# Kernel tuning notes

Measured on AMD Instinct MI355X. Metric: run time of the kernel, lower is better.

The kernel has to match this reference:

```python
import jax, jax.numpy as jnp
import numpy as np

B, S, P, E, H, FF = 4, 16, 256, 768, 12, 3072
HD = E // H
LN_EPS = 1e-5


def _layernorm(x, g, b):
    m = jnp.mean(x, axis=-1, keepdims=True)
    v = jnp.mean((x - m) ** 2, axis=-1, keepdims=True)
    return (x - m) * jax.lax.rsqrt(v + LN_EPS) * g + b


def _qkv(x, wqkv, bqkv):
    # wqkv: [3, E, E] (in, out layout), bqkv: [3, E]
    qkv = jnp.einsum('bspe,tef->tbspf', x, wqkv) + bqkv[:, None, None, None, :]
    q, k, v = qkv
    b, s, p, e = x.shape
    shp = (b, s, p, H, HD)
    return q.reshape(shp), k.reshape(shp), v.reshape(shp)


def spatial_attn(x, wqkv, bqkv, wo, bo, g, beta):
    q, k, v = _qkv(x, wqkv, bqkv)  # [b,s,p,n,d]
    scale = 1.0 / np.sqrt(HD).astype(np.float32)
    scores = jnp.einsum('bsind,bsjnd->bsnij', q, k) * scale  # [b,s,n,p,p]
    attn = jax.nn.softmax(scores, axis=-1)
    out = jnp.einsum('bsnij,bsjnd->bsind', attn, v)  # [b,s,p,n,d]
    out = out.reshape(x.shape)
    out = out @ wo + bo
    return _layernorm(x + out, g, beta)


def temporal_attn(x, wqkv, bqkv, wo, bo, g, beta):
    q, k, v = _qkv(x, wqkv, bqkv)  # [b,s,p,n,d]
    scale = 1.0 / np.sqrt(HD).astype(np.float32)
    scores = jnp.einsum('bipnd,bjpnd->bpnij', q, k) * scale  # [b,p,n,s,s]
    s = x.shape[1]
    causal = jnp.tril(jnp.ones((s, s), dtype=bool))
    scores = jnp.where(causal, scores, jnp.float32(-jnp.inf))
    attn = jax.nn.softmax(scores, axis=-1)
    out = jnp.einsum('bpnij,bjpnd->bipnd', attn, v)  # [b,s,p,n,d]
    out = out.reshape(x.shape)
    out = out @ wo + bo
    return _layernorm(x + out, g, beta)


def ffn(x, w1, b1, w2, b2, g, beta):
    h = jax.nn.relu(x @ w1 + b1)
    out = h @ w2 + b2
    return _layernorm(x + out, g, beta)


def setup_inputs() -> dict:
    key = jax.random.key(0)
    ks = jax.random.split(key, 16)
    w = lambda k, shp: (jax.random.normal(k, shp, dtype=jnp.float32) * 0.02)
    inp = {
        'x': jax.random.normal(ks[0], (B, S, P, E), dtype=jnp.float32),
        'sa_wqkv': w(ks[1], (3, E, E)), 'sa_bqkv': jnp.zeros((3, E), jnp.float32),
        'sa_wo': w(ks[2], (E, E)), 'sa_bo': jnp.zeros((E,), jnp.float32),
        'sa_g': jnp.ones((E,), jnp.float32), 'sa_b': jnp.zeros((E,), jnp.float32),
        'ta_wqkv': w(ks[3], (3, E, E)), 'ta_bqkv': jnp.zeros((3, E), jnp.float32),
        'ta_wo': w(ks[4], (E, E)), 'ta_bo': jnp.zeros((E,), jnp.float32),
        'ta_g': jnp.ones((E,), jnp.float32), 'ta_b': jnp.zeros((E,), jnp.float32),
        'f_w1': w(ks[5], (E, FF)), 'f_b1': jnp.zeros((FF,), jnp.float32),
        'f_w2': w(ks[6], (FF, E)), 'f_b2': jnp.zeros((E,), jnp.float32),
        'f_g': jnp.ones((E,), jnp.float32), 'f_b': jnp.zeros((E,), jnp.float32),
    }
    return inp


def reference(x, sa_wqkv, sa_bqkv, sa_wo, sa_bo, sa_g, sa_b,
              ta_wqkv, ta_bqkv, ta_wo, ta_bo, ta_g, ta_b,
              f_w1, f_b1, f_w2, f_b2, f_g, f_b):
    x = spatial_attn(x, sa_wqkv, sa_bqkv, sa_wo, sa_bo, sa_g, sa_b)
    x = temporal_attn(x, ta_wqkv, ta_bqkv, ta_wo, ta_bo, ta_g, ta_b)
    x = ffn(x, f_w1, f_b1, f_w2, f_b2, f_g, f_b)
    return x
```

## Files before the change

kernel.cpp:

```cpp
#include <hip/hip_runtime.h>
#include <hip/hip_bf16.h>
#include <math.h>

constexpr int Bc = 4, Sc = 16, Pc = 256, Ec = 768, Hc = 12, HDc = 64, FFc = 3072;
constexpr int Mrows = Bc * Sc * Pc;
constexpr size_t ME = (size_t)Mrows * Ec;

typedef __attribute__((ext_vector_type(4))) float f32x4;
typedef __attribute__((ext_vector_type(8))) short s16x8;
typedef __attribute__((ext_vector_type(4))) short s16x4;

__device__ __forceinline__ short f2bf(float f) {
  union { float f; unsigned u; } v; v.f = f;
  unsigned r = (v.u + 0x7FFFu + ((v.u >> 16) & 1u)) >> 16;
  return (short)r;
}
__device__ __forceinline__ float bf2f(short s) {
  union { unsigned u; float f; } v; v.u = ((unsigned)(unsigned short)s) << 16;
  return v.f;
}

__device__ __forceinline__ void async16(const void* g, void* l) {
  __builtin_amdgcn_global_load_lds(
      (const __attribute__((address_space(1))) unsigned int*)g,
      (__attribute__((address_space(3))) unsigned int*)l, 16, 0, 0);
}

__device__ __forceinline__ void wtrans_tile(const float* __restrict__ W,
                                            short* __restrict__ Wt,
                                            int K, int N, int n0, int k0, int t)
{
  const int n  = n0 + (t >> 2);
  const int kc = k0 + (t & 3) * 16;
  short buf[16];
#pragma unroll
  for (int i = 0; i < 16; ++i)
    buf[i] = f2bf(W[(size_t)(kc + i) * N + n]);
  *reinterpret_cast<s16x8*>(&Wt[(size_t)n * K + kc])     = *reinterpret_cast<s16x8*>(&buf[0]);
  *reinterpret_cast<s16x8*>(&Wt[(size_t)n * K + kc + 8]) = *reinterpret_cast<s16x8*>(&buf[8]);
}

__global__ __launch_bounds__(256)
void prep_kernel(const float* __restrict__ x, short* __restrict__ Xb,
                 const float* __restrict__ saqkv, short* __restrict__ wt_saqkv,
                 const float* __restrict__ sawo,  short* __restrict__ wt_sawo,
                 const float* __restrict__ taqkv, short* __restrict__ wt_taqkv,
                 const float* __restrict__ tawo,  short* __restrict__ wt_tawo,
                 const float* __restrict__ fw1,   short* __restrict__ wt_fw1,
                 const float* __restrict__ fw2,   short* __restrict__ wt_fw2)
{
  const int b = blockIdx.x;
  const int t = threadIdx.x;
  constexpr size_t EE = (size_t)Ec * Ec;

  if (b < 432) {
    const int z = b / 144, tl = b % 144;
    wtrans_tile(saqkv + (size_t)z * EE, wt_saqkv + (size_t)z * EE,
                Ec, Ec, (tl % 12) * 64, (tl / 12) * 64, t);
  } else if (b < 576) {
    const int tl = b - 432;
    wtrans_tile(sawo, wt_sawo, Ec, Ec, (tl % 12) * 64, (tl / 12) * 64, t);
  } else if (b < 1008) {
    const int z = (b - 576) / 144, tl = (b - 576) % 144;
    wtrans_tile(taqkv + (size_t)z * EE, wt_taqkv + (size_t)z * EE,
                Ec, Ec, (tl % 12) * 64, (tl / 12) * 64, t);
  } else if (b < 1152) {
    const int tl = b - 1008;
    wtrans_tile(tawo, wt_tawo, Ec, Ec, (tl % 12) * 64, (tl / 12) * 64, t);
  } else if (b < 1728) {
    const int tl = b - 1152;
    wtrans_tile(fw1, wt_fw1, Ec, FFc, (tl % 48) * 64, (tl / 48) * 64, t);
  } else if (b < 2304) {
    const int tl = b - 1728;
    wtrans_tile(fw2, wt_fw2, FFc, Ec, (tl % 12) * 64, (tl / 12) * 64, t);
  } else {
    const size_t i = (size_t)(b - 2304) * 256 + t;
    const float4* p = reinterpret_cast<const float4*>(x + i * 8);
    float4 a = p[0], bb = p[1];
    s16x8 o = { f2bf(a.x), f2bf(a.y), f2bf(a.z), f2bf(a.w),
                f2bf(bb.x), f2bf(bb.y), f2bf(bb.z), f2bf(bb.w) };
    *reinterpret_cast<s16x8*>(Xb + i * 8) = o;
  }
}

#define LDFRAG(base, row, kc) \
  (*reinterpret_cast<const s16x8*>((base) + (row) * 128 + ((((kc) ^ ((row) & 7)) << 4))))

#define PH_READS(Aslot, Bslot, q, LDB) \
  do { \
    if (LDB) { \
      _Pragma("unroll") \
      for (int nj = 0; nj < 4; ++nj) { \
        bfr[nj][0] = LDFRAG((Bslot), wc * 64 + nj * 16 + l16, g); \
        bfr[nj][1] = LDFRAG((Bslot), wc * 64 + nj * 16 + l16, 4 + g); \
      } \
    } \
    _Pragma("unroll") \
    for (int mi = 0; mi < 2; ++mi) { \
      const int arow = wr * 128 + ((q) * 2 + mi) * 16 + l16; \
      afr[mi][0] = LDFRAG((Aslot), arow, g); \
      afr[mi][1] = LDFRAG((Aslot), arow, 4 + g); \
    } \
  } while (0)

#define PH_SYNC_MMA(q) \
  do { \
    __builtin_amdgcn_sched_barrier(0); \
    __builtin_amdgcn_s_barrier(); \
    asm volatile("s_waitcnt lgkmcnt(0)" ::: "memory"); \
    __builtin_amdgcn_sched_barrier(0); \
    __builtin_amdgcn_s_setprio(1); \
    _Pragma("unroll") \
    for (int mi = 0; mi < 2; ++mi) \
      _Pragma("unroll") \
      for (int nj = 0; nj < 4; ++nj) { \
        acc[(q) * 2 + mi][nj] = __builtin_amdgcn_mfma_f32_16x16x32_bf16( \
            afr[mi][0], bfr[nj][0], acc[(q) * 2 + mi][nj], 0, 0, 0); \
        acc[(q) * 2 + mi][nj] = __builtin_amdgcn_mfma_f32_16x16x32_bf16( \
            afr[mi][1], bfr[nj][1], acc[(q) * 2 + mi][nj], 0, 0, 0); \
      } \
    __builtin_amdgcn_s_setprio(0); \
  } while (0)

#define PH_END \
  do { __builtin_amdgcn_s_barrier(); __builtin_amdgcn_sched_barrier(0); } while (0)

#define PH_END_VM \
  do { \
    asm volatile("s_waitcnt vmcnt(4)" ::: "memory"); \
    __builtin_amdgcn_sched_barrier(0); \
    __builtin_amdgcn_s_barrier(); \
    __builtin_amdgcn_sched_barrier(0); \
  } while (0)

template<int OUT>
__global__ __launch_bounds__(512, 2)
void gemm256_kernel(const short* __restrict__ A, const short* __restrict__ Wt,
                    const float* __restrict__ biasg, const void* __restrict__ resv,
                    void* __restrict__ Cg, short* __restrict__ vt,
                    int M, int N, int K)
{
  __shared__ char smem[131072];
  const int z = blockIdx.z;
  const short* __restrict__ Wz = Wt + (size_t)z * (size_t)N * K;
  const float* __restrict__ bz = biasg + (size_t)z * N;

  const int nwg = gridDim.x;
  const int swz = ((int)blockIdx.x & 7) * (nwg >> 3) + ((int)blockIdx.x >> 3);
  const int NT = N >> 8;
  const int bm = (swz / NT) << 8;
  const int bn = (swz % NT) << 8;

  const int tid  = threadIdx.x;
  const int lane = tid & 63;
  const int wid  = tid >> 6;
  const int wr   = wid >> 2;
  const int wc   = wid & 3;
  const int l16  = lane & 15;
  const int g    = lane >> 4;

  char* const As0 = smem;
  char* const Bs0 = smem + 32768;
  char* const As1 = smem + 65536;
  char* const Bs1 = smem + 98304;

  const int srow = lane >> 3;
  const int scol = ((lane & 7) ^ srow) * 8;
  const int ldso = wid * 1024;

  auto stageG = [&](const short* __restrict__ G, int grow0, int k0, char* ldsHalf) {
    const size_t r0 = (size_t)(grow0 + wid * 8 + srow);
    async16(G + r0 * K + (k0 + scol), ldsHalf + ldso);
    async16(G + (r0 + 64) * K + (k0 + scol), ldsHalf + 8192 + ldso);
  };

  f32x4 acc[8][4];
  s16x8 bfr[4][2];
  s16x8 afr[2][2];
#pragma unroll
  for (int mi = 0; mi < 8; ++mi)
#pragma unroll
    for (int nj = 0; nj < 4; ++nj) acc[mi][nj] = f32x4{0.f, 0.f, 0.f, 0.f};

  const int ntile = K >> 6;
  const int nit   = ntile >> 1;

  stageG(A,  bm,        0,  As0);
  stageG(A,  bm + 128,  0,  As0 + 16384);
  stageG(Wz, bn,        0,  Bs0);
  stageG(Wz, bn + 128,  0,  Bs0 + 16384);
  stageG(Wz, bn,        64, Bs1);
  stageG(Wz, bn + 128,  64, Bs1 + 16384);
  asm volatile("s_waitcnt vmcnt(4)" ::: "memory");
  __builtin_amdgcn_sched_barrier(0);
  __builtin_amdgcn_s_barrier();

  for (int j = 0; j < nit; ++j) {
    const int t1k = (2 * j + 1) << 6;
    const int t2k = (2 * j + 2) << 6;
    const int t3k = (2 * j + 3) << 6;
    const bool s2 = (2 * j + 2) < ntile;
    const bool s3 = (2 * j + 3) < ntile;

    PH_READS(As0, Bs0, 0, true);
    stageG(A, bm, t1k, As1);
    PH_SYNC_MMA(0);
    PH_END;

    PH_READS(As0, Bs0, 1, false);
    stageG(A, bm + 128, t1k, As1 + 16384);
    PH_SYNC_MMA(1);
    PH_END;

    PH_READS(As0, Bs0, 2, false);
    if (s2) stageG(Wz, bn, t2k, Bs0);
    PH_SYNC_MMA(2);
    PH_END;

    PH_READS(As0, Bs0, 3, false);
    if (s2) stageG(Wz, bn + 128, t2k, Bs0 + 16384);
    PH_SYNC_MMA(3);
    PH_END_VM;

    PH_READS(As1, Bs1, 0, true);
    if (s2) stageG(A, bm, t2k, As0);
    PH_SYNC_MMA(0);
    PH_END;

    PH_READS(As1, Bs1, 1, false);
    if (s2) stageG(A, bm + 128, t2k, As0 + 16384);
    PH_SYNC_MMA(1);
    PH_END;

    PH_READS(As1, Bs1, 2, false);
    if (s3) stageG(Wz, bn, t3k, Bs1);
    PH_SYNC_MMA(2);
    PH_END;

    PH_READS(As1, Bs1, 3, false);
    if (s3) stageG(Wz, bn + 128, t3k, Bs1 + 16384);
    PH_SYNC_MMA(3);
    PH_END_VM;
  }

  const short* resb = (const short*)resv;
  short* Cb = (short*)Cg + (size_t)z * (size_t)M * N;

#pragma unroll
  for (int mi = 0; mi < 8; ++mi) {
    const int row0 = bm + wr * 128 + mi * 16 + g * 4;
#pragma unroll
    for (int nj = 0; nj < 4; ++nj) {
      const int col = bn + wc * 64 + nj * 16 + l16;
      if (OUT == 4 && z == 2) {
        const int bs2 = row0 >> 8, p0 = row0 & 255;
        const int h2 = col >> 6,  d2 = col & 63;
        const float bias = bz[col];
        s16x4 v = { f2bf(acc[mi][nj][0] + bias), f2bf(acc[mi][nj][1] + bias),
                    f2bf(acc[mi][nj][2] + bias), f2bf(acc[mi][nj][3] + bias) };
        *reinterpret_cast<s16x4*>(
            &vt[(((size_t)bs2 * 12 + h2) * 64 + d2) * 256 + p0]) = v;
      } else {
        const float bias = bz[col];
#pragma unroll
        for (int r = 0; r < 4; ++r) {
          float v = acc[mi][nj][r] + bias;
          size_t idx = (size_t)(row0 + r) * N + col;
          if (OUT == 3) v += bf2f(resb[idx]);
          if (OUT == 1) v = fmaxf(v, 0.f);
          Cb[idx] = f2bf(v);
        }
      }
    }
  }
}

__global__ __launch_bounds__(256, 3)
void spatial_attn_kernel(const short* __restrict__ Qg, const short* __restrict__ Kg,
                         const short* __restrict__ Vt, short* __restrict__ Og)
{
  const int bs = blockIdx.x;
  const int h  = blockIdx.y;

  __shared__ short Pl[4 * 32 * 64];

  const int tid  = threadIdx.x;
  const int lane = tid & 63;
  const int wid  = tid >> 6;
  const int l16  = lane & 15;
  const int g    = lane >> 4;
  const int q0   = blockIdx.z * 128 + wid * 32;
  char* Pw = (char*)Pl + wid * 4096;

  const size_t rowbase = (size_t)(bs * 256) * 768 + h * 64;
  const size_t vbase   = ((size_t)bs * 12 + h) * 64 * 256;

  s16x8 qa[2][2];
#pragma unroll
  for (int m = 0; m < 2; ++m)
#pragma unroll
    for (int ks = 0; ks < 2; ++ks)
      qa[m][ks] = *reinterpret_cast<const s16x8*>(
          &Qg[rowbase + (size_t)(q0 + m * 16 + l16) * 768 + ks * 32 + g * 8]);

  float mrun[2][4], lrun[2][4];
  f32x4 oac[2][4];
#pragma unroll
  for (int m = 0; m < 2; ++m)
#pragma unroll
    for (int r = 0; r < 4; ++r) { mrun[m][r] = -INFINITY; lrun[m][r] = 0.f; }
#pragma unroll
  for (int m = 0; m < 2; ++m)
#pragma unroll
    for (int n = 0; n < 4; ++n) oac[m][n] = f32x4{0.f, 0.f, 0.f, 0.f};

#pragma unroll
  for (int t = 0; t < 4; ++t) {
    const int key0 = t * 64;
    f32x4 sc[2][4];
#pragma unroll
    for (int m = 0; m < 2; ++m)
#pragma unroll
      for (int n = 0; n < 4; ++n) sc[m][n] = f32x4{0.f, 0.f, 0.f, 0.f};
#pragma unroll
    for (int ks = 0; ks < 2; ++ks) {
      s16x8 kf[4];
#pragma unroll
      for (int n = 0; n < 4; ++n) {
        const int key = key0 + n * 16 + l16;
        kf[n] = *reinterpret_cast<const s16x8*>(
            &Kg[rowbase + (size_t)key * 768 + ks * 32 + g * 8]);
      }
#pragma unroll
      for (int m = 0; m < 2; ++m)
#pragma unroll
        for (int n = 0; n < 4; ++n)
          sc[m][n] = __builtin_amdgcn_mfma_f32_16x16x32_bf16(qa[m][ks], kf[n], sc[m][n], 0, 0, 0);
    }
#pragma unroll
    for (int m = 0; m < 2; ++m)
#pragma unroll
      for (int n = 0; n < 4; ++n)
#pragma unroll
        for (int r = 0; r < 4; ++r) sc[m][n][r] *= 0.125f;

#pragma unroll
    for (int m = 0; m < 2; ++m) {
#pragma unroll
      for (int r = 0; r < 4; ++r) {
        float mx = fmaxf(fmaxf(sc[m][0][r], sc[m][1][r]), fmaxf(sc[m][2][r], sc[m][3][r]));
#pragma unroll
        for (int mk = 1; mk < 16; mk <<= 1) mx = fmaxf(mx, __shfl_xor(mx, mk, 64));
        const float mnew = fmaxf(mrun[m][r], mx);
        const float corr = __expf(mrun[m][r] - mnew);
        mrun[m][r] = mnew;
        float rs = 0.f;
#pragma unroll
        for (int n = 0; n < 4; ++n) {
          float p = __expf(sc[m][n][r] - mnew);
          sc[m][n][r] = p;
          rs += p;
        }
#pragma unroll
        for (int mk = 1; mk < 16; mk <<= 1) rs += __shfl_xor(rs, mk, 64);
        lrun[m][r] = lrun[m][r] * corr + rs;
#pragma unroll
        for (int nd = 0; nd < 4; ++nd) oac[m][nd][r] *= corr;
      }
    }
#pragma unroll
    for (int m = 0; m < 2; ++m)
#pragma unroll
      for (int n = 0; n < 4; ++n)
#pragma unroll
        for (int r = 0; r < 4; ++r) {
          const int q = m * 16 + g * 4 + r;
          const int key = n * 16 + l16;
          const int byte = q * 128 + (((key >> 3) ^ (q & 7)) * 16) + (key & 7) * 2;
          *reinterpret_cast<short*>(Pw + byte) = f2bf(sc[m][n][r]);
        }
#pragma unroll
    for (int ks = 0; ks < 2; ++ks) {
      s16x8 pa[2], vf[4];
#pragma unroll
      for (int m = 0; m < 2; ++m) {
        const int q = m * 16 + l16;
        const int s = ks * 4 + g;
        pa[m] = *reinterpret_cast<const s16x8*>(Pw + q * 128 + ((s ^ (q & 7)) * 16));
      }
#pragma unroll
      for (int nd = 0; nd < 4; ++nd) {
        const int d = nd * 16 + l16;
        const int key = key0 + ks * 32 + g * 8;
        vf[nd] = *reinterpret_cast<const s16x8*>(&Vt[vbase + (size_t)d * 256 + key]);
      }
#pragma unroll
      for (int m = 0; m < 2; ++m)
#pragma unroll
        for (int nd = 0; nd < 4; ++nd)
          oac[m][nd] = __builtin_amdgcn_mfma_f32_16x16x32_bf16(pa[m], vf[nd], oac[m][nd], 0, 0, 0);
    }
  }

#pragma unroll
  for (int m = 0; m < 2; ++m)
#pragma unroll
    for (int r = 0; r < 4; ++r) {
      const float inv = 1.f / lrun[m][r];
#pragma unroll
      for (int nd = 0; nd < 4; ++nd) oac[m][nd][r] *= inv;
    }
#pragma unroll
  for (int m = 0; m < 2; ++m)
#pragma unroll
    for (int nd = 0; nd < 4; ++nd)
#pragma unroll
      for (int r = 0; r < 4; ++r) {
        const int q = m * 16 + g * 4 + r;
        const int d = nd * 16 + l16;
        const int byte = q * 128 + (((d >> 3) ^ (q & 7)) * 16) + (d & 7) * 2;
        *reinterpret_cast<short*>(Pw + byte) = f2bf(oac[m][nd][r]);
      }
#pragma unroll
  for (int it = 0; it < 4; ++it) {
    const int slot = it * 64 + lane;
    const int q = slot >> 3, sl = slot & 7;
    const int d0 = (sl ^ (q & 7)) * 8;
    s16x8 v = *reinterpret_cast<const s16x8*>(Pw + slot * 16);
    *reinterpret_cast<s16x8*>(
        &Og[rowbase + (size_t)(q0 + q) * 768 + d0]) = v;
  }
}

__global__ __launch_bounds__(192)
void temporal_attn_kernel(const short* __restrict__ Qg, const short* __restrict__ Kg,
                          const short* __restrict__ Vg, short* __restrict__ Og)
{
  const int bp = blockIdx.x;
  const int b = bp >> 8, p = bp & 255;

  __shared__ short Ks[16 * 768];
  __shared__ short Vs[16 * 768];

  const int tid = threadIdx.x;
  const size_t gbase = ((size_t)(b * 16) * 256 + p) * 768;
  constexpr int SROW = 256 * 768;

  {
    const int half = tid / 96;
    const int cc   = tid - half * 96;
    const int c    = cc & 7, hs = cc >> 3;
    const int ldso = (c * 12 + hs) * 8;
#pragma unroll
    for (int it = 0; it < 8; ++it) {
      const int s = it * 2 + half;
      const size_t ga = gbase + (size_t)s * SROW + cc * 8;
      *reinterpret_cast<s16x8*>(&Ks[s * 768 + ldso]) =
          *reinterpret_cast<const s16x8*>(&Kg[ga]);
      *reinterpret_cast<s16x8*>(&Vs[s * 768 + ldso]) =
          *reinterpret_cast<const s16x8*>(&Vg[ga]);
    }
  }
  __syncthreads();

  const int h = tid % 12, i = tid / 12;
  const float scale = 0.125f;
  const size_t qoff = gbase + (size_t)i * SROW + h * 64;

  float q[HDc];
#pragma unroll
  for (int c = 0; c < 8; ++c) {
    s16x8 v = *reinterpret_cast<const s16x8*>(&Qg[qoff + c * 8]);
#pragma unroll
    for (int e = 0; e < 8; ++e) q[c * 8 + e] = bf2f(v[e]) * scale;
  }

  float m = -INFINITY, l = 0.f;
  float o[HDc];
#pragma unroll
  for (int d = 0; d < HDc; ++d) o[d] = 0.f;

  for (int j = 0; j <= i; ++j) {
    const short* kr = &Ks[j * 768];
    float s = 0.f;
#pragma unroll
    for (int c = 0; c < 8; ++c) {
      s16x8 kv = *reinterpret_cast<const s16x8*>(kr + (c * 12 + h) * 8);
#pragma unroll
      for (int e = 0; e < 8; ++e) s += q[c * 8 + e] * bf2f(kv[e]);
    }
    float mn   = fmaxf(m, s);
    float corr = __expf(m - mn);
    float pw   = __expf(s - mn);
    l = l * corr + pw;
    const short* vr = &Vs[j * 768];
#pragma unroll
    for (int c = 0; c < 8; ++c) {
      s16x8 vv = *reinterpret_cast<const s16x8*>(vr + (c * 12 + h) * 8);
#pragma unroll
      for (int e = 0; e < 8; ++e)
        o[c * 8 + e] = fmaf(pw, bf2f(vv[e]), o[c * 8 + e] * corr);
    }
    m = mn;
  }
  const float inv = 1.f / l;
  short* op = &Og[qoff];
#pragma unroll
  for (int c = 0; c < 8; ++c) {
    s16x8 v;
#pragma unroll
    for (int e = 0; e < 8; ++e) v[e] = f2bf(o[c * 8 + e] * inv);
    *reinterpret_cast<s16x8*>(op + c * 8) = v;
  }
}

template<bool OUTBF>
__global__ __launch_bounds__(256)
void layernorm_kernel(const short* __restrict__ U, const float* __restrict__ g,
                      const float* __restrict__ be, void* __restrict__ outv)
{
  const int tid  = threadIdx.x;
  const int lane = tid & 63, w = tid >> 6;
  const size_t row = (size_t)blockIdx.x * 4 + w;
  const short* u = U + row * Ec;

  float x[12];
#pragma unroll
  for (int c = 0; c < 3; ++c) {
    s16x4 v = *reinterpret_cast<const s16x4*>(&u[c * 256 + lane * 4]);
    x[c*4+0] = bf2f(v[0]); x[c*4+1] = bf2f(v[1]);
    x[c*4+2] = bf2f(v[2]); x[c*4+3] = bf2f(v[3]);
  }
  float s = 0.f;
#pragma unroll
  for (int k = 0; k < 12; ++k) s += x[k];
#pragma unroll
  for (int off = 32; off > 0; off >>= 1) s += __shfl_xor(s, off, 64);
  const float mean = s * (1.f / 768.f);

  float vs = 0.f;
#pragma unroll
  for (int k = 0; k < 12; ++k) { float d = x[k] - mean; vs += d * d; }
#pragma unroll
  for (int off = 32; off > 0; off >>= 1) vs += __shfl_xor(vs, off, 64);
  const float rs = rsqrtf(vs * (1.f / 768.f) + 1e-5f);

#pragma unroll
  for (int c = 0; c < 3; ++c) {
    int idx = c * 256 + lane * 4;
    float4 gv = *reinterpret_cast<const float4*>(&g[idx]);
    float4 bv = *reinterpret_cast<const float4*>(&be[idx]);
    float r0 = (x[c*4+0] - mean) * rs * gv.x + bv.x;
    float r1 = (x[c*4+1] - mean) * rs * gv.y + bv.y;
    float r2 = (x[c*4+2] - mean) * rs * gv.z + bv.z;
    float r3 = (x[c*4+3] - mean) * rs * gv.w + bv.w;
    if (OUTBF) {
      short* op = (short*)outv + row * Ec + idx;
      s16x4 v = { f2bf(r0), f2bf(r1), f2bf(r2), f2bf(r3) };
      *reinterpret_cast<s16x4*>(op) = v;
    } else {
      float* op = (float*)outv + row * Ec + idx;
      *reinterpret_cast<float4*>(op) = make_float4(r0, r1, r2, r3);
    }
  }
}

extern "C" void kernel_launch(void* const* d_in, const int* in_sizes, int n_in,
                              void* d_out, int out_size, void* d_ws, size_t ws_size,
                              hipStream_t stream)
{
  const float* x       = (const float*)d_in[0];
  const float* sa_wqkv = (const float*)d_in[1];
  const float* sa_bqkv = (const float*)d_in[2];
  const float* sa_wo   = (const float*)d_in[3];
  const float* sa_bo   = (const float*)d_in[4];
  const float* sa_g    = (const float*)d_in[5];
  const float* sa_b    = (const float*)d_in[6];
  const float* ta_wqkv = (const float*)d_in[7];
  const float* ta_bqkv = (const float*)d_in[8];
  const float* ta_wo   = (const float*)d_in[9];
  const float* ta_bo   = (const float*)d_in[10];
  const float* ta_g    = (const float*)d_in[11];
  const float* ta_b    = (const float*)d_in[12];
  const float* f_w1    = (const float*)d_in[13];
  const float* f_b1    = (const float*)d_in[14];
  const float* f_w2    = (const float*)d_in[15];
  const float* f_b2    = (const float*)d_in[16];
  const float* f_g     = (const float*)d_in[17];
  const float* f_b     = (const float*)d_in[18];

  float* out = (float*)d_out;

  constexpr size_t EE = (size_t)Ec * Ec;
  constexpr size_t WTOT = 3*EE + EE + 3*EE + EE + 2*(size_t)Ec*FFc;
  const size_t need = 12 * ME + 2 * WTOT;
  if (ws_size < need) return;

  short* Xb  = (short*)d_ws;
  short* Qb  = Xb + ME;
  short* Kb  = Qb + ME;
  short* Vtb = Qb + 2 * ME;
  short* Hb  = Qb;
  short* U   = Xb + 5 * ME;
  short* Wtb = U + ME;

  short* wt_sa_qkv = Wtb;
  short* wt_sa_wo  = wt_sa_qkv + 3 * EE;
  short* wt_ta_qkv = wt_sa_wo  + EE;
  short* wt_ta_wo  = wt_ta_qkv + 3 * EE;
  short* wt_f_w1   = wt_ta_wo  + EE;
  short* wt_f_w2   = wt_f_w1   + (size_t)Ec * FFc;

  prep_kernel<<<8448, 256, 0, stream>>>(
      x, Xb, sa_wqkv, wt_sa_qkv, sa_wo, wt_sa_wo,
      ta_wqkv, wt_ta_qkv, ta_wo, wt_ta_wo, f_w1, wt_f_w1, f_w2, wt_f_w2);

  const dim3 gQKV((Mrows / 256) * (Ec / 256), 1, 3);
  const dim3 gSQ ((Mrows / 256) * (Ec / 256), 1, 1);
  const dim3 gFF1((Mrows / 256) * (FFc / 256), 1, 1);

  gemm256_kernel<4><<<gQKV, 512, 0, stream>>>(Xb, wt_sa_qkv, sa_bqkv, nullptr, Qb, Vtb, Mrows, Ec, Ec);
  spatial_attn_kernel<<<dim3(Bc * Sc, Hc, 2), 256, 0, stream>>>(Qb, Kb, Vtb, Qb);
  gemm256_kernel<3><<<gSQ, 512, 0, stream>>>(Qb, wt_sa_wo, sa_bo, Xb, U, nullptr, Mrows, Ec, Ec);
  layernorm_kernel<true><<<Mrows / 4, 256, 0, stream>>>(U, sa_g, sa_b, Xb);

  gemm256_kernel<0><<<gQKV, 512, 0, stream>>>(Xb, wt_ta_qkv, ta_bqkv, nullptr, Qb, nullptr, Mrows, Ec, Ec);
  temporal_attn_kernel<<<Bc * Pc, 192, 0, stream>>>(Qb, Kb, Vtb, Qb);
  gemm256_kernel<3><<<gSQ, 512, 0, stream>>>(Qb, wt_ta_wo, ta_bo, Xb, U, nullptr, Mrows, Ec, Ec);
  layernorm_kernel<true><<<Mrows / 4, 256, 0, stream>>>(U, ta_g, ta_b, Xb);

  gemm256_kernel<1><<<gFF1, 512, 0, stream>>>(Xb, wt_f_w1, f_b1, nullptr, Hb, nullptr, Mrows, FFc, Ec);
  gemm256_kernel<3><<<gSQ, 512, 0, stream>>>(Hb, wt_f_w2, f_b2, Xb, U, nullptr, Mrows, Ec, FFc);
  layernorm_kernel<false><<<Mrows / 4, 256, 0, stream>>>(U, f_g, f_b, out);
}
```

Before: 562.3 us.

## Add 256x192-tile GEMM for N=768 projections to fill all CUs

Introduces a gemm192 kernel that tiles the output as 256x192, with a three-phase per-K-tile pipeline and B staging of 192 rows. All N=768 GEMMs (QKV, output projections, FFN down) use it, so the grid grows from 192 to 256 workgroups per projection and covers more compute units. The tail waitcnt also becomes conditional and drains fully on the last tile. In exchange, per-tile reuse is lower and register pressure changes because each wave now computes 8x3 fragments.

Measured after the change: 529.0 us. 5.9% less time.

```diff
diff --git a/kernel.cpp b/kernel.cpp
--- a/kernel.cpp
+++ b/kernel.cpp
@@ -86,6 +86,29 @@
 #define LDFRAG(base, row, kc) \
   (*reinterpret_cast<const s16x8*>((base) + (row) * 128 + ((((kc) ^ ((row) & 7)) << 4))))
 
+#define PH_BAR_MMA_BEGIN \
+  do { \
+    __builtin_amdgcn_sched_barrier(0); \
+    __builtin_amdgcn_s_barrier(); \
+    asm volatile("s_waitcnt lgkmcnt(0)" ::: "memory"); \
+    __builtin_amdgcn_sched_barrier(0); \
+    __builtin_amdgcn_s_setprio(1); \
+  } while (0)
+
+#define PH_END \
+  do { __builtin_amdgcn_s_setprio(0); __builtin_amdgcn_s_barrier(); \
+       __builtin_amdgcn_sched_barrier(0); } while (0)
+
+#define PH_END_VMC(cond, nstr) \
+  do { \
+    __builtin_amdgcn_s_setprio(0); \
+    if (cond) asm volatile("s_waitcnt vmcnt(" nstr ")" ::: "memory"); \
+    else      asm volatile("s_waitcnt vmcnt(0)" ::: "memory"); \
+    __builtin_amdgcn_sched_barrier(0); \
+    __builtin_amdgcn_s_barrier(); \
+    __builtin_amdgcn_sched_barrier(0); \
+  } while (0)
+
 #define PH_READS(Aslot, Bslot, q, LDB) \
   do { \
     if (LDB) { \
@@ -103,13 +126,9 @@
     } \
   } while (0)
 
-#define PH_SYNC_MMA(q) \
+#define PH_MMA4(q) \
   do { \
-    __builtin_amdgcn_sched_barrier(0); \
-    __builtin_amdgcn_s_barrier(); \
-    asm volatile("s_waitcnt lgkmcnt(0)" ::: "memory"); \
-    __builtin_amdgcn_sched_barrier(0); \
-    __builtin_amdgcn_s_setprio(1); \
+    PH_BAR_MMA_BEGIN; \
     _Pragma("unroll") \
     for (int mi = 0; mi < 2; ++mi) \
       _Pragma("unroll") \
@@ -119,18 +138,6 @@
         acc[(q) * 2 + mi][nj] = __builtin_amdgcn_mfma_f32_16x16x32_bf16( \
             afr[mi][1], bfr[nj][1], acc[(q) * 2 + mi][nj], 0, 0, 0); \
       } \
-    __builtin_amdgcn_s_setprio(0); \
-  } while (0)
-
-#define PH_END \
-  do { __builtin_amdgcn_s_barrier(); __builtin_amdgcn_sched_barrier(0); } while (0)
-
-#define PH_END_VM \
-  do { \
-    asm volatile("s_waitcnt vmcnt(4)" ::: "memory"); \
-    __builtin_amdgcn_sched_barrier(0); \
-    __builtin_amdgcn_s_barrier(); \
-    __builtin_amdgcn_sched_barrier(0); \
   } while (0)
 
 template<int OUT>
@@ -204,43 +211,185 @@
 
     PH_READS(As0, Bs0, 0, true);
     stageG(A, bm, t1k, As1);
-    PH_SYNC_MMA(0);
-    PH_END;
+    PH_MMA4(0); PH_END;
 
     PH_READS(As0, Bs0, 1, false);
     stageG(A, bm + 128, t1k, As1 + 16384);
-    PH_SYNC_MMA(1);
-    PH_END;
+    PH_MMA4(1); PH_END;
 
     PH_READS(As0, Bs0, 2, false);
     if (s2) stageG(Wz, bn, t2k, Bs0);
-    PH_SYNC_MMA(2);
-    PH_END;
+    PH_MMA4(2); PH_END;
 
     PH_READS(As0, Bs0, 3, false);
     if (s2) stageG(Wz, bn + 128, t2k, Bs0 + 16384);
-    PH_SYNC_MMA(3);
-    PH_END_VM;
+    PH_MMA4(3); PH_END_VMC(s2, "4");
 
     PH_READS(As1, Bs1, 0, true);
     if (s2) stageG(A, bm, t2k, As0);
-    PH_SYNC_MMA(0);
-    PH_END;
+    PH_MMA4(0); PH_END;
 
     PH_READS(As1, Bs1, 1, false);
     if (s2) stageG(A, bm + 128, t2k, As0 + 16384);
-    PH_SYNC_MMA(1);
-    PH_END;
+    PH_MMA4(1); PH_END;
 
     PH_READS(As1, Bs1, 2, false);
     if (s3) stageG(Wz, bn, t3k, Bs1);
-    PH_SYNC_MMA(2);
-    PH_END;
+    PH_MMA4(2); PH_END;
 
     PH_READS(As1, Bs1, 3, false);
     if (s3) stageG(Wz, bn + 128, t3k, Bs1 + 16384);
-    PH_SYNC_MMA(3);
-    PH_END_VM;
+    PH_MMA4(3); PH_END_VMC(s3, "4");
+  }
+
+  short* Cb = (short*)Cg + (size_t)z * (size_t)M * N;
+#pragma unroll
+  for (int mi = 0; mi < 8; ++mi) {
+    const int row0 = bm + wr * 128 + mi * 16 + g * 4;
+#pragma unroll
+    for (int nj = 0; nj < 4; ++nj) {
+      const int col = bn + wc * 64 + nj * 16 + l16;
+      const float bias = bz[col];
+#pragma unroll
+      for (int r = 0; r < 4; ++r) {
+        float v = acc[mi][nj][r] + bias;
+        size_t idx = (size_t)(row0 + r) * N + col;
+        if (OUT == 1) v = fmaxf(v, 0.f);
+        Cb[idx] = f2bf(v);
+      }
+    }
+  }
+}
+
+#define R_READ_A(Aslot, m0, mcnt) \
+  do { \
+    _Pragma("unroll") \
+    for (int mi = (m0); mi < (m0) + (mcnt); ++mi) { \
+      const int arow = wr * 128 + mi * 16 + l16; \
+      afr[mi][0] = LDFRAG((Aslot), arow, g); \
+      afr[mi][1] = LDFRAG((Aslot), arow, 4 + g); \
+    } \
+  } while (0)
+
+#define R_READ_B(Bslot) \
+  do { \
+    _Pragma("unroll") \
+    for (int nj = 0; nj < 3; ++nj) { \
+      const int brow = wc * 48 + nj * 16 + l16; \
+      bfr[nj][0] = LDFRAG((Bslot), brow, g); \
+      bfr[nj][1] = LDFRAG((Bslot), brow, 4 + g); \
+    } \
+  } while (0)
+
+#define R_MMA(p) \
+  do { \
+    PH_BAR_MMA_BEGIN; \
+    _Pragma("unroll") \
+    for (int pi = 8 * (p); pi < 8 * (p) + 8; ++pi) { \
+      const int mi = pi / 3, nj = pi % 3; \
+      acc[mi][nj] = __builtin_amdgcn_mfma_f32_16x16x32_bf16( \
+          afr[mi][0], bfr[nj][0], acc[mi][nj], 0, 0, 0); \
+      acc[mi][nj] = __builtin_amdgcn_mfma_f32_16x16x32_bf16( \
+          afr[mi][1], bfr[nj][1], acc[mi][nj], 0, 0, 0); \
+    } \
+  } while (0)
+
+template<int OUT>
+__global__ __launch_bounds__(512, 2)
+void gemm192_kernel(const short* __restrict__ A, const short* __restrict__ Wt,
+                    const float* __restrict__ biasg, const void* __restrict__ resv,
+                    void* __restrict__ Cg, short* __restrict__ vt,
+                    int M, int N, int K)
+{
+  __shared__ char smem[114688];
+  const int z = blockIdx.z;
+  const short* __restrict__ Wz = Wt + (size_t)z * (size_t)N * K;
+  const float* __restrict__ bz = biasg + (size_t)z * N;
+
+  const int nwg = gridDim.x;
+  const int swz = ((int)blockIdx.x & 7) * (nwg >> 3) + ((int)blockIdx.x >> 3);
+  const int NT = N / 192;
+  const int bm = (swz / NT) << 8;
+  const int bn = (swz % NT) * 192;
+
+  const int tid  = threadIdx.x;
+  const int lane = tid & 63;
+  const int wid  = tid >> 6;
+  const int wr   = wid >> 2;
+  const int wc   = wid & 3;
+  const int l16  = lane & 15;
+  const int g    = lane >> 4;
+
+  char* const As0 = smem;
+  char* const As1 = smem + 32768;
+  char* const Bs0 = smem + 65536;
+  char* const Bs1 = smem + 90112;
+
+  const int srow = lane >> 3;
+  const int scol = ((lane & 7) ^ srow) * 8;
+  const int ldso = wid * 1024;
+
+  auto stageG = [&](const short* __restrict__ G, int grow0, int k0, char* ldsHalf) {
+    const size_t r0 = (size_t)(grow0 + wid * 8 + srow);
+    async16(G + r0 * K + (k0 + scol), ldsHalf + ldso);
+    async16(G + (r0 + 64) * K + (k0 + scol), ldsHalf + 8192 + ldso);
+  };
+  auto stageB = [&](const short* __restrict__ G, int grow0, int k0, char* ldsB) {
+    const size_t r0 = (size_t)(grow0 + wid * 8 + srow);
+    async16(G + r0 * K + (k0 + scol), ldsB + ldso);
+    async16(G + (r0 + 64) * K + (k0 + scol), ldsB + 8192 + ldso);
+    async16(G + (r0 + 128) * K + (k0 + scol), ldsB + 16384 + ldso);
+  };
+
+  f32x4 acc[8][3];
+  s16x8 afr[8][2];
+  s16x8 bfr[3][2];
+#pragma unroll
+  for (int mi = 0; mi < 8; ++mi)
+#pragma unroll
+    for (int nj = 0; nj < 3; ++nj) acc[mi][nj] = f32x4{0.f, 0.f, 0.f, 0.f};
+
+  const int ntile = K >> 6;
+  const int nit   = ntile >> 1;
+
+  stageG(A,  bm,       0,  As0);
+  stageG(A,  bm + 128, 0,  As0 + 16384);
+  stageB(Wz, bn,       0,  Bs0);
+  stageB(Wz, bn,       64, Bs1);
+  asm volatile("s_waitcnt vmcnt(3)" ::: "memory");
+  __builtin_amdgcn_sched_barrier(0);
+  __builtin_amdgcn_s_barrier();
+
+  for (int j = 0; j < nit; ++j) {
+    const int t1k = (2 * j + 1) << 6;
+    const int t2k = (2 * j + 2) << 6;
+    const int t3k = (2 * j + 3) << 6;
+    const bool s2 = (2 * j + 2) < ntile;
+    const bool s3 = (2 * j + 3) < ntile;
+
+    R_READ_A(As0, 0, 3); R_READ_B(Bs0);
+    stageG(A, bm, t1k, As1);
+    R_MMA(0); PH_END;
+
+    R_READ_A(As0, 3, 3);
+    stageG(A, bm + 128, t1k, As1 + 16384);
+    R_MMA(1); PH_END;
+
+    R_READ_A(As0, 6, 2);
+    if (s2) stageB(Wz, bn, t2k, Bs0);
+    R_MMA(2); PH_END_VMC(s2, "3");
+
+    R_READ_A(As1, 0, 3); R_READ_B(Bs1);
+    if (s2) stageG(A, bm, t2k, As0);
+    R_MMA(0); PH_END;
+
+    R_READ_A(As1, 3, 3);
+    if (s2) stageG(A, bm + 128, t2k, As0 + 16384);
+    R_MMA(1); PH_END;
+
+    R_READ_A(As1, 6, 2);
+    if (s3) stageB(Wz, bn, t3k, Bs1);
+    R_MMA(2); PH_END_VMC(s3, "3");
   }
 
   const short* resb = (const short*)resv;
@@ -250,8 +399,8 @@
   for (int mi = 0; mi < 8; ++mi) {
     const int row0 = bm + wr * 128 + mi * 16 + g * 4;
 #pragma unroll
-    for (int nj = 0; nj < 4; ++nj) {
-      const int col = bn + wc * 64 + nj * 16 + l16;
+    for (int nj = 0; nj < 3; ++nj) {
+      const int col = bn + wc * 48 + nj * 16 + l16;
       if (OUT == 4 && z == 2) {
         const int bs2 = row0 >> 8, p0 = row0 & 255;
         const int h2 = col >> 6,  d2 = col & 63;
@@ -267,7 +416,6 @@
           float v = acc[mi][nj][r] + bias;
           size_t idx = (size_t)(row0 + r) * N + col;
           if (OUT == 3) v += bf2f(resb[idx]);
-          if (OUT == 1) v = fmaxf(v, 0.f);
           Cb[idx] = f2bf(v);
         }
       }
@@ -615,21 +763,21 @@
       x, Xb, sa_wqkv, wt_sa_qkv, sa_wo, wt_sa_wo,
       ta_wqkv, wt_ta_qkv, ta_wo, wt_ta_wo, f_w1, wt_f_w1, f_w2, wt_f_w2);
 
-  const dim3 gQKV((Mrows / 256) * (Ec / 256), 1, 3);
-  const dim3 gSQ ((Mrows / 256) * (Ec / 256), 1, 1);
+  const dim3 gQKV((Mrows / 256) * (Ec / 192), 1, 3);
+  const dim3 gSQ ((Mrows / 256) * (Ec / 192), 1, 1);
   const dim3 gFF1((Mrows / 256) * (FFc / 256), 1, 1);
 
-  gemm256_kernel<4><<<gQKV, 512, 0, stream>>>(Xb, wt_sa_qkv, sa_bqkv, nullptr, Qb, Vtb, Mrows, Ec, Ec);
+  gemm192_kernel<4><<<gQKV, 512, 0, stream>>>(Xb, wt_sa_qkv, sa_bqkv, nullptr, Qb, Vtb, Mrows, Ec, Ec);
   spatial_attn_kernel<<<dim3(Bc * Sc, Hc, 2), 256, 0, stream>>>(Qb, Kb, Vtb, Qb);
-  gemm256_kernel<3><<<gSQ, 512, 0, stream>>>(Qb, wt_sa_wo, sa_bo, Xb, U, nullptr, Mrows, Ec, Ec);
+  gemm192_kernel<3><<<gSQ, 512, 0, stream>>>(Qb, wt_sa_wo, sa_bo, Xb, U, nullptr, Mrows, Ec, Ec);
   layernorm_kernel<true><<<Mrows / 4, 256, 0, stream>>>(U, sa_g, sa_b, Xb);
 
-  gemm256_kernel<0><<<gQKV, 512, 0, stream>>>(Xb, wt_ta_qkv, ta_bqkv, nullptr, Qb, nullptr, Mrows, Ec, Ec);
+  gemm192_kernel<0><<<gQKV, 512, 0, stream>>>(Xb, wt_ta_qkv, ta_bqkv, nullptr, Qb, nullptr, Mrows, Ec, Ec);
   temporal_attn_kernel<<<Bc * Pc, 192, 0, stream>>>(Qb, Kb, Vtb, Qb);
-  gemm256_kernel<3><<<gSQ, 512, 0, stream>>>(Qb, wt_ta_wo, ta_bo, Xb, U, nullptr, Mrows, Ec, Ec);
+  gemm192_kernel<3><<<gSQ, 512, 0, stream>>>(Qb, wt_ta_wo, ta_bo, Xb, U, nullptr, Mrows, Ec, Ec);
   layernorm_kernel<true><<<Mrows / 4, 256, 0, stream>>>(U, ta_g, ta_b, Xb);
 
   gemm256_kernel<1><<<gFF1, 512, 0, stream>>>(Xb, wt_f_w1, f_b1, nullptr, Hb, nullptr, Mrows, FFc, Ec);
-  gemm256_kernel<3><<<gSQ, 512, 0, stream>>>(Hb, wt_f_w2, f_b2, Xb, U, nullptr, Mrows, Ec, FFc);
+  gemm192_kernel<3><<<gSQ, 512, 0, stream>>>(Hb, wt_f_w2, f_b2, Xb, U, nullptr, Mrows, Ec, FFc);
   layernorm_kernel<false><<<Mrows / 4, 256, 0, stream>>>(U, f_g, f_b, out);
 }
```
